# Optimization experiments

Hardware: AMD Instinct MI355X
Metric: run time of the kernel (lower is better)

Reference implementation:

```python
import jax, jax.numpy as jnp
import numpy as np

B, T, H = 8, 2048, 1024
F = 4096
E = 8
TOP_K = 2


def setup_inputs() -> dict:
    key = jax.random.key(0)
    ks = jax.random.split(key, 6)
    s_h = 1.0 / np.sqrt(H)
    s_f = 1.0 / np.sqrt(F)
    return {
        "hidden_states": jax.random.normal(ks[0], (B, T, H), dtype=jnp.float32),
        "gate_w": jax.random.uniform(ks[1], (H, E), minval=-s_h, maxval=s_h, dtype=jnp.float32),
        "w1": jax.random.uniform(ks[2], (E, H, F), minval=-s_h, maxval=s_h, dtype=jnp.float32),
        "b1": jax.random.uniform(ks[3], (E, F), minval=-s_h, maxval=s_h, dtype=jnp.float32),
        "w2": jax.random.uniform(ks[4], (E, F, H), minval=-s_f, maxval=s_f, dtype=jnp.float32),
        "b2": jax.random.uniform(ks[5], (E, H), minval=-s_f, maxval=s_f, dtype=jnp.float32),
    }


def reference(hidden_states, gate_w, w1, b1, w2, b2):
    b, t, h = hidden_states.shape
    # Sequence-level routing: mean over tokens -> gate logits
    seq_rep = hidden_states.mean(axis=1)                       # [B, H]
    router_logits = seq_rep @ gate_w                           # [B, E]
    probs = jax.nn.softmax(router_logits.astype(jnp.float32), axis=-1)
    top_w, top_i = jax.lax.top_k(probs, TOP_K)                 # [B, K]
    top_w = top_w / top_w.sum(axis=-1, keepdims=True)
    top_w = top_w.astype(hidden_states.dtype)
    # Dense combine weights [B, E] (zero for unselected experts)
    combine = jnp.zeros((b, E), dtype=hidden_states.dtype)
    combine = combine.at[jnp.arange(b)[:, None], top_i].set(top_w)
    out = jnp.zeros_like(hidden_states)
    for e in range(E):  # small fixed expert loop
        hmid = jax.nn.gelu(jnp.einsum("bth,hf->btf", hidden_states, w1[e]) + b1[e],
                           approximate=False)
        y = jnp.einsum("btf,fh->bth", hmid, w2[e]) + b2[e]
        out = out + combine[:, e][:, None, None] * y
    return out
```

## Files before the change

kernel.cpp:

```cpp
#include <hip/hip_runtime.h>
#include <hip/hip_bf16.h>
#include <math.h>

#define BB 8
#define TT 2048
#define HH 1024
#define FF 4096
#define EE 8

typedef __attribute__((ext_vector_type(8))) short sh8;
typedef __attribute__((ext_vector_type(4))) short sh4;
typedef __attribute__((ext_vector_type(4))) float f32x4;
typedef __attribute__((ext_vector_type(4))) float f4;

__device__ inline unsigned short f2bf(float f) {
  unsigned u = __builtin_bit_cast(unsigned, f);
  u += 0x7FFFu + ((u >> 16) & 1u);
  return (unsigned short)(u >> 16);
}

__device__ inline float erf_fast(float x) {
  float ax = fabsf(x);
  float t = 1.0f / (1.0f + 0.3275911f * ax);
  float y = t * (0.254829592f +
           t * (-0.284496736f +
           t * (1.421413741f +
           t * (-1.453152027f +
           t * 1.061405429f))));
  float e = __expf(-ax * ax);
  float r = 1.0f - y * e;
  return copysignf(r, x);
}

__device__ inline void gload_lds16(const void* g, void* l) {
  __builtin_amdgcn_global_load_lds(
      (const __attribute__((address_space(1))) unsigned int*)g,
      (__attribute__((address_space(3))) unsigned int*)l, 16, 0, 0);
}

__global__ __launch_bounds__(256) void prep(const float* __restrict__ X,
                                            unsigned short* __restrict__ Xb,
                                            float* __restrict__ partial) {
  int tc = blockIdx.x, b = blockIdx.y, t = threadIdx.x;
  const float* src = X + ((size_t)b * TT + (size_t)tc * 128) * HH;
  unsigned short* dst = Xb + ((size_t)b * TT + (size_t)tc * 128) * HH;
  f4 s = {0.f, 0.f, 0.f, 0.f};
  for (int r = 0; r < 128; ++r) {
    f4 v = *(const f4*)&src[(size_t)r * HH + t * 4];
    s[0] += v[0]; s[1] += v[1]; s[2] += v[2]; s[3] += v[3];
    sh4 o;
    o[0] = (short)f2bf(v[0]); o[1] = (short)f2bf(v[1]);
    o[2] = (short)f2bf(v[2]); o[3] = (short)f2bf(v[3]);
    *(sh4*)&dst[(size_t)r * HH + t * 4] = o;
  }
  *(f4*)&partial[((size_t)b * 16 + tc) * HH + t * 4] = s;
}

__global__ __launch_bounds__(256) void gating_kernel(const float* __restrict__ partial,
                                                     const float* __restrict__ gw,
                                                     int* __restrict__ re,
                                                     float* __restrict__ rw) {
  int b = blockIdx.x, t = threadIdx.x;
  float acc[EE];
#pragma unroll
  for (int e = 0; e < EE; e++) acc[e] = 0.f;
  for (int jj = 0; jj < 4; jj++) {
    int h = t + jj * 256;
    float s = 0.f;
    for (int tc = 0; tc < 16; tc++) s += partial[((size_t)b * 16 + tc) * HH + h];
    s *= (1.0f / (float)TT);
#pragma unroll
    for (int e = 0; e < EE; e++) acc[e] += s * gw[h * EE + e];
  }
#pragma unroll
  for (int off = 32; off >= 1; off >>= 1) {
#pragma unroll
    for (int e = 0; e < EE; e++) acc[e] += __shfl_down(acc[e], off);
  }
  __shared__ float red[4][EE];
  if ((t & 63) == 0) {
#pragma unroll
    for (int e = 0; e < EE; e++) red[t >> 6][e] = acc[e];
  }
  __syncthreads();
  if (t == 0) {
    float lg[EE];
#pragma unroll
    for (int e = 0; e < EE; e++) lg[e] = red[0][e] + red[1][e] + red[2][e] + red[3][e];
    float mx = lg[0];
#pragma unroll
    for (int e = 1; e < EE; e++) mx = fmaxf(mx, lg[e]);
    float p[EE]; float s = 0.f;
#pragma unroll
    for (int e = 0; e < EE; e++) { p[e] = expf(lg[e] - mx); s += p[e]; }
#pragma unroll
    for (int e = 0; e < EE; e++) p[e] /= s;
    int i1 = 0;
#pragma unroll
    for (int e = 1; e < EE; e++) if (p[e] > p[i1]) i1 = e;
    int i2 = -1;
#pragma unroll
    for (int e = 0; e < EE; e++) {
      if (e == i1) continue;
      if (i2 < 0 || p[e] > p[i2]) i2 = e;
    }
    float den = p[i1] + p[i2];
    re[b * 2 + 0] = i1; rw[b * 2 + 0] = p[i1] / den;
    re[b * 2 + 1] = i2; rw[b * 2 + 1] = p[i2] / den;
  }
}

__global__ __launch_bounds__(256) void transposeE(const float* __restrict__ W,
                                                  unsigned short* __restrict__ Wt,
                                                  const int* __restrict__ re,
                                                  int K, int N) {
  int e = blockIdx.z;
  bool u = false;
#pragma unroll
  for (int p = 0; p < 16; p++) u = u || (re[p] == e);
  if (!u) return;

  __shared__ float tile[64][65];
  int kb = blockIdx.x, nb = blockIdx.y;
  const float* src = W + (size_t)e * K * N + (size_t)(kb * 64) * N + nb * 64;
  int t = threadIdx.x;
#pragma unroll
  for (int pass = 0; pass < 4; pass++) {
    int r = (t >> 4) + pass * 16;
    int c = (t & 15) * 4;
    *(f4*)&tile[r][c] = *(const f4*)&src[(size_t)r * N + c];
  }
  __syncthreads();
#pragma unroll
  for (int pass = 0; pass < 2; pass++) {
    int idx = (t + pass * 256) * 8;
    int nl = idx >> 6, k0 = idx & 63;
    sh8 o;
#pragma unroll
    for (int j = 0; j < 8; j++) o[j] = (short)f2bf(tile[k0 + j][nl]);
    *(sh8*)&Wt[(size_t)e * N * K + (size_t)(nb * 64 + nl) * K + kb * 64 + k0] = o;
  }
}


#define MFMA_CL(qm, qn, BREG)                                                      \
    __builtin_amdgcn_s_setprio(1);                                                 \
    _Pragma("unroll")                                                              \
    for (int m4 = 0; m4 < 4; m4++)                                                 \
      _Pragma("unroll")                                                            \
      for (int n2 = 0; n2 < 2; n2++)                                               \
        _Pragma("unroll")                                                          \
        for (int kk = 0; kk < 2; kk++)                                             \
          acc[(qm) * 4 + m4][(qn) * 2 + n2] =                                      \
              __builtin_amdgcn_mfma_f32_16x16x32_bf16(                             \
                  Aq[m4 * 2 + kk], BREG[n2 * 2 + kk],                              \
                  acc[(qm) * 4 + m4][(qn) * 2 + n2], 0, 0, 0);                     \
    __builtin_amdgcn_s_setprio(0);

#define PH_PRE                                                                     \
    __builtin_amdgcn_sched_barrier(0);                                             \
    __builtin_amdgcn_s_barrier();                                                  \
    asm volatile("s_waitcnt lgkmcnt(0)" ::: "memory");                             \
    __builtin_amdgcn_sched_barrier(0);

#define PH_POST(VM)                                                                \
    if ((VM) == 4) { asm volatile("s_waitcnt vmcnt(4)" ::: "memory"); }            \
    else if ((VM) == 1) { asm volatile("s_waitcnt vmcnt(0)" ::: "memory"); }       \
    __builtin_amdgcn_sched_barrier(0);                                             \
    __builtin_amdgcn_s_barrier();

#define PH1(buf, STMT, VM) do {                                                    \
    _Pragma("unroll")                                                              \
    for (int m4 = 0; m4 < 4; m4++) {                                               \
      Aq[m4 * 2]     = *(const sh8*)(pA0 + (buf) * 32768 + m4 * 2048);             \
      Aq[m4 * 2 + 1] = *(const sh8*)(pA1 + (buf) * 32768 + m4 * 2048);             \
    }                                                                              \
    _Pragma("unroll")                                                              \
    for (int n2 = 0; n2 < 2; n2++) {                                               \
      B0r[n2 * 2]     = *(const sh8*)(pB0 + (buf) * 32768 + n2 * 2048);            \
      B0r[n2 * 2 + 1] = *(const sh8*)(pB1 + (buf) * 32768 + n2 * 2048);            \
    }                                                                              \
    STMT; PH_PRE MFMA_CL(0, 0, B0r) PH_POST(VM) } while (0)

#define PH2(buf, STMT, VM) do {                                                    \
    _Pragma("unroll")                                                              \
    for (int n2 = 0; n2 < 2; n2++) {                                               \
      B1r[n2 * 2]     = *(const sh8*)(pB0 + (buf) * 32768 + 4096 + n2 * 2048);     \
      B1r[n2 * 2 + 1] = *(const sh8*)(pB1 + (buf) * 32768 + 4096 + n2 * 2048);     \
    }                                                                              \
    STMT; PH_PRE MFMA_CL(0, 1, B1r) PH_POST(VM) } while (0)

#define PH3(buf, STMT, VM) do {                                                    \
    _Pragma("unroll")                                                              \
    for (int m4 = 0; m4 < 4; m4++) {                                               \
      Aq[m4 * 2]     = *(const sh8*)(pA0 + (buf) * 32768 + 8192 + m4 * 2048);      \
      Aq[m4 * 2 + 1] = *(const sh8*)(pA1 + (buf) * 32768 + 8192 + m4 * 2048);      \
    }                                                                              \
    STMT; PH_PRE MFMA_CL(1, 1, B1r) PH_POST(VM) } while (0)

#define PH4(buf, STMT, VM) do {                                                    \
    STMT; PH_PRE MFMA_CL(1, 0, B0r) PH_POST(VM) } while (0)

#define STAGE_A(tau, q) do {                                                       \
    int bo_ = ((tau) & 1) * 32768;                                                 \
    if constexpr (MODE == 0) {                                                     \
      const unsigned short* ap_ = A0p + ((tau) & 15) * 64;                         \
      gload_lds16(ap_ + oA##q##0, lds + lA + bo_ + (q) * 8192);                    \
      gload_lds16(ap_ + oA##q##1, lds + lA + bo_ + (q) * 8192 + 16384);            \
    } else {                                                                       \
      int kt_ = ((tau) < NTH) ? (tau) : (tau) - NTH;                               \
      const unsigned short* ap_ = (((tau) < NTH) ? H0p : H1p) +                    \
                                  (kt_ >> 2) * 65536 + (kt_ & 3) * 8192;           \
      gload_lds16(ap_ + fA##q##0, lds + lA + bo_ + (q) * 8192);                    \
      gload_lds16(ap_ + fA##q##1, lds + lA + bo_ + (q) * 8192 + 16384);            \
    } } while (0)

#define STAGE_B(tau, q) do {                                                       \
    int bo_ = ((tau) & 1) * 32768;                                                 \
    if constexpr (MODE == 0) {                                                     \
      const unsigned short* bp_ = w1tE +                                           \
          (size_t)(nbh8 + ((tau) >> 4)) * (256 * HH) + ((tau) & 15) * 64;          \
      gload_lds16(bp_ + oB##q##0, lds + lB + bo_ + (q) * 4096);                    \
      gload_lds16(bp_ + oB##q##1, lds + lB + bo_ + (q) * 4096 + 16384);            \
    } else {                                                                       \
      int kt_ = ((tau) < NTH) ? (tau) : (tau) - NTH;                               \
      const unsigned short* bp_ = (((tau) < NTH) ? B0p : B1p) + kt_ * 64;          \
      gload_lds16(bp_ + oB##q##0, lds + lB + bo_ + (q) * 4096);                    \
      gload_lds16(bp_ + oB##q##1, lds + lB + bo_ + (q) * 4096 + 16384);            \
    } } while (0)

#define STD8(T)                                                                    \
    PH1(0, { STAGE_A((T) + 1, 1); }, 0);                                           \
    PH2(0, { STAGE_B((T) + 1, 1); }, 0);                                           \
    PH3(0, { STAGE_A((T) + 2, 0); }, 0);                                           \
    PH4(0, { STAGE_B((T) + 2, 0); }, 4);                                           \
    PH1(1, { STAGE_A((T) + 2, 1); }, 0);                                           \
    PH2(1, { STAGE_B((T) + 2, 1); }, 0);                                           \
    PH3(1, { STAGE_A((T) + 3, 0); }, 0);                                           \
    PH4(1, { STAGE_B((T) + 3, 0); }, 4);

#define TAIL8(T)                                                                   \
    PH1(0, { STAGE_A((T) + 1, 1); }, 0);                                           \
    PH2(0, { STAGE_B((T) + 1, 1); }, 0);                                           \
    PH3(0, {}, 0);                                                                 \
    PH4(0, {}, 1);                                                                 \
    PH1(1, {}, 0);                                                                 \
    PH2(1, {}, 0);                                                                 \
    PH3(1, {}, 0);                                                                 \
    PH4(1, {}, 0);

template <int MODE>
__global__ __launch_bounds__(512, 1) void gemm8p(
    const unsigned short* __restrict__ XorH,
    const unsigned short* __restrict__ Wt,
    const float* __restrict__ bias,
    const int* __restrict__ re,
    const float* __restrict__ rw,
    unsigned short* __restrict__ hmid_out,
    float* __restrict__ out) {
  extern __shared__ char lds[];

  constexpr int NT  = 128;
  constexpr int NTH = (MODE == 0) ? NT : (FF / 64);

  int P = blockIdx.x;
  int t = threadIdx.x;
  int lane = t & 63, wv = t >> 6;
  int wr = wv >> 2, wc = wv & 3;
  int ln = lane & 15, kq = lane >> 4;

  const unsigned short *A0p = nullptr, *w1tE = nullptr;
  const unsigned short *H0p = nullptr, *H1p = nullptr, *B0p = nullptr, *B1p = nullptr;
  int pair = 0, b, e0 = 0, e1 = 0, mb, nb = 0, nbh8 = 0;
  int ldb;
  if constexpr (MODE == 0) {
    b = P & 7;
    int k = P >> 3;
    int pairbit = k & 1;
    mb = (k >> 1) & 7;
    nbh8 = (k >> 4) * 8;
    pair = b * 2 + pairbit;
    e0 = re[pair];
    A0p = XorH + (size_t)b * TT * HH + (size_t)mb * 256 * HH;
    w1tE = Wt + (size_t)e0 * FF * HH;
    ldb = HH;
  } else {
    b = P & 7;
    int idx = P >> 3;
    nb = idx & 3; mb = idx >> 2;
    e0 = re[2 * b]; e1 = re[2 * b + 1];
    H0p = XorH + (size_t)(2 * b) * TT * FF + (size_t)mb * 16 * 65536;
    H1p = H0p + (size_t)TT * FF;
    B0p = Wt + (size_t)e0 * FF * HH + (size_t)nb * 256 * FF;
    B1p = Wt + (size_t)e1 * FF * HH + (size_t)nb * 256 * FF;
    ldb = FF;
  }

  int lrow = t >> 3;
  int lrB8 = (t >> 8) * 64 + ((t >> 3) & 31);
  int clel = ((t & 7) ^ ((t >> 3) & 7)) * 8;
  size_t oA00 = (size_t)(lrow)*HH + clel;
  size_t oA01 = (size_t)(128 + lrow) * HH + clel;
  size_t oA10 = (size_t)(64 + lrow) * HH + clel;
  size_t oA11 = (size_t)(192 + lrow) * HH + clel;
  int nnl = (clel >> 4) & 3, lnl = clel & 15;
#define FPERM(r) ((size_t)((((r) >> 7) & 1) * 32768 +                              \
                  ((((r) >> 4) & 7) * 16 + nnl * 4 + ((r) & 3)) * 64 +             \
                  (((r) >> 2) & 3) * 16 + lnl))
  size_t fA00 = FPERM(lrow);
  size_t fA01 = FPERM(128 + lrow);
  size_t fA10 = FPERM(64 + lrow);
  size_t fA11 = FPERM(192 + lrow);
#undef FPERM
  size_t oB00 = (size_t)(lrB8)*ldb + clel;
  size_t oB01 = (size_t)(128 + lrB8) * ldb + clel;
  size_t oB10 = (size_t)(32 + lrB8) * ldb + clel;
  size_t oB11 = (size_t)(160 + lrB8) * ldb + clel;
  int lA = lrow * 128 + (t & 7) * 16;
  int lB = 65536 + lrB8 * 128 + (t & 7) * 16;
  char* pA0 = lds + wr * 16384 + ln * 128 + ((kq ^ (ln & 7)) * 16);
  char* pA1 = lds + wr * 16384 + ln * 128 + (((4 + kq) ^ (ln & 7)) * 16);
  char* pB0 = lds + 65536 + wc * 8192 + ln * 128 + ((kq ^ (ln & 7)) * 16);
  char* pB1 = lds + 65536 + wc * 8192 + ln * 128 + (((4 + kq) ^ (ln & 7)) * 16);

  f32x4 acc[8][4];
#pragma unroll
  for (int m = 0; m < 8; m++)
#pragma unroll
    for (int n = 0; n < 4; n++) acc[m][n] = (f32x4){0.f, 0.f, 0.f, 0.f};

  sh8 Aq[8], B0r[4], B1r[4];

  STAGE_A(0, 0); STAGE_B(0, 0); STAGE_A(0, 1); STAGE_B(0, 1);
  STAGE_A(1, 0); STAGE_B(1, 0);
  asm volatile("s_waitcnt vmcnt(4)" ::: "memory");
  __builtin_amdgcn_sched_barrier(0);
  __builtin_amdgcn_s_barrier();

  if constexpr (MODE == 0) {
    float wgt = rw[pair];
    for (int seg = 0; seg < 8; ++seg) {
      int nIt = (seg == 7) ? 7 : 8;
      for (int it = 0; it < nIt; ++it) {
        int T = seg * 16 + it * 2;
        STD8(T);
      }
      if (seg == 7) { TAIL8(126); }
      {
        int nbs = nbh8 + seg;
        float bbv[4];
#pragma unroll
        for (int nn = 0; nn < 4; nn++)
          bbv[nn] = bias[(size_t)e0 * FF + nbs * 256 + wc * 64 + nn * 16 + ln];
        unsigned short* Cp = hmid_out + (size_t)pair * TT * FF +
                             (size_t)(mb * 16 + nbs) * 65536 + wv * 8192 + lane;
#pragma unroll
        for (int mm = 0; mm < 8; mm++) {
#pragma unroll
          for (int nn = 0; nn < 4; nn++) {
#pragma unroll
            for (int j = 0; j < 4; j++) {
              float v = acc[mm][nn][j] + bbv[nn];
              float g = 0.5f * v * (1.0f + erf_fast(v * 0.70710678118654752f));
              __builtin_nontemporal_store(f2bf(wgt * g),
                                          Cp + (mm * 16 + nn * 4 + j) * 64);
            }
          }
        }
#pragma unroll
        for (int m = 0; m < 8; m++)
#pragma unroll
          for (int n = 0; n < 4; n++) acc[m][n] = (f32x4){0.f, 0.f, 0.f, 0.f};
      }
    }
  } else {
    for (int T = 0; T + 2 < NT; T += 2) {
      STD8(T);
    }
    TAIL8(NT - 2);
    float w0 = rw[2 * b], w1v = rw[2 * b + 1];
#pragma unroll
    for (int nn = 0; nn < 4; nn++) {
      int col = nb * 256 + wc * 64 + nn * 16 + ln;
      float bv = w0 * bias[(size_t)e0 * HH + col] + w1v * bias[(size_t)e1 * HH + col];
#pragma unroll
      for (int mm = 0; mm < 8; mm++) {
#pragma unroll
        for (int j = 0; j < 4; j++) {
          int row = mb * 256 + wr * 128 + mm * 16 + kq * 4 + j;
          __builtin_nontemporal_store(acc[mm][nn][j] + bv,
              &out[(size_t)b * TT * HH + (size_t)row * HH + col]);
        }
      }
    }
  }
}

extern "C" void kernel_launch(void* const* d_in, const int* in_sizes, int n_in,
                              void* d_out, int out_size, void* d_ws, size_t ws_size,
                              hipStream_t stream) {
  const float* X  = (const float*)d_in[0];
  const float* gw = (const float*)d_in[1];
  const float* w1 = (const float*)d_in[2];
  const float* pb1 = (const float*)d_in[3];
  const float* w2 = (const float*)d_in[4];
  const float* pb2 = (const float*)d_in[5];
  float* out = (float*)d_out;

  char* ws = (char*)d_ws;
  int* re = (int*)ws;
  float* rw = (float*)(ws + 64);
  float* partial = (float*)(ws + 256);
  unsigned short* Xbf = (unsigned short*)(ws + 256 + 524288);
  const size_t fixed = 256 + 524288 + (size_t)BB * TT * HH * 2;

  unsigned short* w1t = (unsigned short*)(ws + fixed);
  unsigned short* w2t = (unsigned short*)(ws + fixed + (size_t)EE * HH * FF * 2);
  unsigned short* hmid = (unsigned short*)(ws + fixed + (size_t)2 * EE * HH * FF * 2);

  hipFuncSetAttribute((const void*)gemm8p<0>,
                      hipFuncAttributeMaxDynamicSharedMemorySize, 131072);
  hipFuncSetAttribute((const void*)gemm8p<1>,
                      hipFuncAttributeMaxDynamicSharedMemorySize, 131072);

  prep<<<dim3(16, BB), 256, 0, stream>>>(X, Xbf, partial);
  gating_kernel<<<BB, 256, 0, stream>>>(partial, gw, re, rw);

  transposeE<<<dim3(HH / 64, FF / 64, EE), 256, 0, stream>>>(w1, w1t, re, HH, FF);
  transposeE<<<dim3(FF / 64, HH / 64, EE), 256, 0, stream>>>(w2, w2t, re, FF, HH);

  gemm8p<0><<<256, 512, 131072, stream>>>(Xbf, w1t, pb1, re, rw, hmid, nullptr);
  gemm8p<1><<<256, 512, 131072, stream>>>(hmid, w2t, pb2, re, rw, nullptr, out);
}
```

Measured before the change: 641.5 us.

## Overlap GELU epilogue of previous segment with first MFMA phases of next

Measured after the change: 947.5 us. 47.7% more time.

```diff
diff --git a/kernel.cpp b/kernel.cpp
--- a/kernel.cpp
+++ b/kernel.cpp
@@ -157,6 +157,36 @@
                   acc[(qm) * 4 + m4][(qn) * 2 + n2], 0, 0, 0);                     \
     __builtin_amdgcn_s_setprio(0);
 
+#define MFMA_CLZ(qm, qn, BREG)                                                     \
+    __builtin_amdgcn_s_setprio(1);                                                 \
+    _Pragma("unroll")                                                              \
+    for (int m4 = 0; m4 < 4; m4++)                                                 \
+      _Pragma("unroll")                                                            \
+      for (int n2 = 0; n2 < 2; n2++) {                                             \
+        f32x4 z0 = {0.f, 0.f, 0.f, 0.f};                                           \
+        z0 = __builtin_amdgcn_mfma_f32_16x16x32_bf16(                              \
+            Aq[m4 * 2], BREG[n2 * 2], z0, 0, 0, 0);                                \
+        acc[(qm) * 4 + m4][(qn) * 2 + n2] =                                        \
+            __builtin_amdgcn_mfma_f32_16x16x32_bf16(                               \
+                Aq[m4 * 2 + 1], BREG[n2 * 2 + 1], z0, 0, 0, 0);                    \
+      }                                                                            \
+    __builtin_amdgcn_s_setprio(0);
+
+#define EPI_SLICE(qm, qn) do {                                                     \
+    _Pragma("unroll")                                                              \
+    for (int m4 = 0; m4 < 4; m4++)                                                 \
+      _Pragma("unroll")                                                            \
+      for (int n2 = 0; n2 < 2; n2++)                                               \
+        _Pragma("unroll")                                                          \
+        for (int j = 0; j < 4; j++) {                                              \
+          int mm_ = (qm) * 4 + m4, nn_ = (qn) * 2 + n2;                            \
+          float v_ = acc[mm_][nn_][j] + bbvP[nn_];                                 \
+          float g_ = 0.5f * v_ * (1.0f + erf_fast(v_ * 0.70710678118654752f));     \
+          __builtin_nontemporal_store(f2bf(wgt * g_),                              \
+                                      CpP + (mm_ * 16 + nn_ * 4 + j) * 64);        \
+        }                                                                          \
+  } while (0)
+
 #define PH_PRE                                                                     \
     __builtin_amdgcn_sched_barrier(0);                                             \
     __builtin_amdgcn_s_barrier();                                                  \
@@ -166,40 +196,40 @@
 #define PH_POST(VM)                                                                \
     if ((VM) == 4) { asm volatile("s_waitcnt vmcnt(4)" ::: "memory"); }            \
     else if ((VM) == 1) { asm volatile("s_waitcnt vmcnt(0)" ::: "memory"); }       \
+    else if ((VM) == 36) { asm volatile("s_waitcnt vmcnt(36)" ::: "memory"); }     \
     __builtin_amdgcn_sched_barrier(0);                                             \
     __builtin_amdgcn_s_barrier();
 
-#define PH1(buf, STMT, VM) do {                                                    \
+#define RD_A(buf, off)                                                             \
     _Pragma("unroll")                                                              \
     for (int m4 = 0; m4 < 4; m4++) {                                               \
-      Aq[m4 * 2]     = *(const sh8*)(pA0 + (buf) * 32768 + m4 * 2048);             \
-      Aq[m4 * 2 + 1] = *(const sh8*)(pA1 + (buf) * 32768 + m4 * 2048);             \
-    }                                                                              \
+      Aq[m4 * 2]     = *(const sh8*)(pA0 + (buf) * 32768 + (off) + m4 * 2048);     \
+      Aq[m4 * 2 + 1] = *(const sh8*)(pA1 + (buf) * 32768 + (off) + m4 * 2048);     \
+    }
+#define RD_B(buf, off, BREG)                                                       \
     _Pragma("unroll")                                                              \
     for (int n2 = 0; n2 < 2; n2++) {                                               \
-      B0r[n2 * 2]     = *(const sh8*)(pB0 + (buf) * 32768 + n2 * 2048);            \
-      B0r[n2 * 2 + 1] = *(const sh8*)(pB1 + (buf) * 32768 + n2 * 2048);            \
-    }                                                                              \
+      BREG[n2 * 2]     = *(const sh8*)(pB0 + (buf) * 32768 + (off) + n2 * 2048);   \
+      BREG[n2 * 2 + 1] = *(const sh8*)(pB1 + (buf) * 32768 + (off) + n2 * 2048);   \
+    }
+
+#define PH1(buf, STMT, VM) do { RD_A(buf, 0) RD_B(buf, 0, B0r)                     \
     STMT; PH_PRE MFMA_CL(0, 0, B0r) PH_POST(VM) } while (0)
-
-#define PH2(buf, STMT, VM) do {                                                    \
-    _Pragma("unroll")                                                              \
-    for (int n2 = 0; n2 < 2; n2++) {                                               \
-      B1r[n2 * 2]     = *(const sh8*)(pB0 + (buf) * 32768 + 4096 + n2 * 2048);     \
-      B1r[n2 * 2 + 1] = *(const sh8*)(pB1 + (buf) * 32768 + 4096 + n2 * 2048);     \
-    }                                                                              \
+#define PH2(buf, STMT, VM) do { RD_B(buf, 4096, B1r)                               \
     STMT; PH_PRE MFMA_CL(0, 1, B1r) PH_POST(VM) } while (0)
-
-#define PH3(buf, STMT, VM) do {                                                    \
-    _Pragma("unroll")                                                              \
-    for (int m4 = 0; m4 < 4; m4++) {                                               \
-      Aq[m4 * 2]     = *(const sh8*)(pA0 + (buf) * 32768 + 8192 + m4 * 2048);      \
-      Aq[m4 * 2 + 1] = *(const sh8*)(pA1 + (buf) * 32768 + 8192 + m4 * 2048);      \
-    }                                                                              \
+#define PH3(buf, STMT, VM) do { RD_A(buf, 8192)                                    \
     STMT; PH_PRE MFMA_CL(1, 1, B1r) PH_POST(VM) } while (0)
-
 #define PH4(buf, STMT, VM) do {                                                    \
     STMT; PH_PRE MFMA_CL(1, 0, B0r) PH_POST(VM) } while (0)
+
+#define PH1Z(buf, STMT, VM) do { RD_A(buf, 0) RD_B(buf, 0, B0r)                    \
+    STMT; PH_PRE MFMA_CLZ(0, 0, B0r) PH_POST(VM) } while (0)
+#define PH2Z(buf, STMT, VM) do { RD_B(buf, 4096, B1r)                              \
+    STMT; PH_PRE MFMA_CLZ(0, 1, B1r) PH_POST(VM) } while (0)
+#define PH3Z(buf, STMT, VM) do { RD_A(buf, 8192)                                   \
+    STMT; PH_PRE MFMA_CLZ(1, 1, B1r) PH_POST(VM) } while (0)
+#define PH4Z(buf, STMT, VM) do {                                                   \
+    STMT; PH_PRE MFMA_CLZ(1, 0, B0r) PH_POST(VM) } while (0)
 
 #define STAGE_A(tau, q) do {                                                       \
     int bo_ = ((tau) & 1) * 32768;                                                 \
@@ -234,6 +264,16 @@
     PH2(0, { STAGE_B((T) + 1, 1); }, 0);                                           \
     PH3(0, { STAGE_A((T) + 2, 0); }, 0);                                           \
     PH4(0, { STAGE_B((T) + 2, 0); }, 4);                                           \
+    PH1(1, { STAGE_A((T) + 2, 1); }, 0);                                           \
+    PH2(1, { STAGE_B((T) + 2, 1); }, 0);                                           \
+    PH3(1, { STAGE_A((T) + 3, 0); }, 0);                                           \
+    PH4(1, { STAGE_B((T) + 3, 0); }, 4);
+
+#define STD8Z(T)                                                                   \
+    PH1Z(0, { EPI_SLICE(0, 0); STAGE_A((T) + 1, 1); }, 0);                         \
+    PH2Z(0, { EPI_SLICE(0, 1); STAGE_B((T) + 1, 1); }, 0);                         \
+    PH3Z(0, { EPI_SLICE(1, 1); STAGE_A((T) + 2, 0); }, 0);                         \
+    PH4Z(0, { EPI_SLICE(1, 0); STAGE_B((T) + 2, 0); }, 36);                        \
     PH1(1, { STAGE_A((T) + 2, 1); }, 0);                                           \
     PH2(1, { STAGE_B((T) + 2, 1); }, 0);                                           \
     PH3(1, { STAGE_A((T) + 3, 0); }, 0);                                           \
@@ -339,39 +379,47 @@
 
   if constexpr (MODE == 0) {
     float wgt = rw[pair];
+    unsigned short* CpP = hmid_out;
+    float bbvP[4] = {0.f, 0.f, 0.f, 0.f};
+    unsigned short* CpC = nullptr;
+    float bbvC[4];
     for (int seg = 0; seg < 8; ++seg) {
-      int nIt = (seg == 7) ? 7 : 8;
-      for (int it = 0; it < nIt; ++it) {
-        int T = seg * 16 + it * 2;
+      int nbs = nbh8 + seg;
+#pragma unroll
+      for (int nn = 0; nn < 4; nn++)
+        bbvC[nn] = bias[(size_t)e0 * FF + nbs * 256 + wc * 64 + nn * 16 + ln];
+      CpC = hmid_out + (size_t)pair * TT * FF +
+            (size_t)(mb * 16 + nbs) * 65536 + wv * 8192 + lane;
+      int T0 = seg * 16;
+      if (seg == 0) {
+        STD8(T0);
+      } else {
+        STD8Z(T0);
+      }
+      int last = (seg == 7) ? 7 : 8;
+      for (int it = 1; it < last; ++it) {
+        int T = T0 + it * 2;
         STD8(T);
       }
-      if (seg == 7) { TAIL8(126); }
-      {
-        int nbs = nbh8 + seg;
-        float bbv[4];
-#pragma unroll
-        for (int nn = 0; nn < 4; nn++)
-          bbv[nn] = bias[(size_t)e0 * FF + nbs * 256 + wc * 64 + nn * 16 + ln];
-        unsigned short* Cp = hmid_out + (size_t)pair * TT * FF +
-                             (size_t)(mb * 16 + nbs) * 65536 + wv * 8192 + lane;
+      if (seg == 7) {
+        TAIL8(126);
 #pragma unroll
         for (int mm = 0; mm < 8; mm++) {
 #pragma unroll
           for (int nn = 0; nn < 4; nn++) {
 #pragma unroll
             for (int j = 0; j < 4; j++) {
-              float v = acc[mm][nn][j] + bbv[nn];
+              float v = acc[mm][nn][j] + bbvC[nn];
               float g = 0.5f * v * (1.0f + erf_fast(v * 0.70710678118654752f));
               __builtin_nontemporal_store(f2bf(wgt * g),
-                                          Cp + (mm * 16 + nn * 4 + j) * 64);
+                                          CpC + (mm * 16 + nn * 4 + j) * 64);
             }
           }
         }
-#pragma unroll
-        for (int m = 0; m < 8; m++)
-#pragma unroll
-          for (int n = 0; n < 4; n++) acc[m][n] = (f32x4){0.f, 0.f, 0.f, 0.f};
       }
+      CpP = CpC;
+#pragma unroll
+      for (int nn = 0; nn < 4; nn++) bbvP[nn] = bbvC[nn];
     }
   } else {
     for (int T = 0; T + 2 < NT; T += 2) {
```
